# Kernel tuning notes

Hardware: AMD Instinct MI355X
Metric: run time of the kernel (lower is better)

## Reference

```python
import jax, jax.numpy as jnp
import numpy as np

N = 100000   # nodes
E = 600000   # edges
G = 64       # graphs in batch
H = 128      # hidden size
F_NODE = 2
F_EDGE = 7
RH = 500     # reghead size
NEG_SLOPE = 0.01
BN_EPS = 1e-5


def leaky(x):
    return jnp.where(x >= 0, x, NEG_SLOPE * x)


def gine_conv(x, src, dst, edge_attr, edge_W, edge_b, W1, b1, gamma, beta, W2, b2):
    # PyG GINEConv: message = ReLU(x_j + Lin(edge_attr)); sum-aggregate at dst;
    # out = nn((1+eps)*x + aggr) with eps=0; nn = Lin -> BN(train) -> LeakyReLU -> Lin -> LeakyReLU
    e = edge_attr @ edge_W.T + edge_b                 # [E, d_in]
    m = jax.nn.relu(x[src] + e)                       # gather + add + relu
    aggr = jax.ops.segment_sum(m, dst, num_segments=N)
    h = x + aggr
    h = h @ W1.T + b1                                 # [N, H]
    mu = jnp.mean(h, axis=0)
    var = jnp.var(h, axis=0)                          # biased, matches BN training
    h = gamma * (h - mu) * jax.lax.rsqrt(var + BN_EPS) + beta
    h = leaky(h)
    h = h @ W2.T + b2
    return leaky(h)


def setup_inputs() -> dict:
    key = jax.random.key(0)
    ks = jax.random.split(key, 24)

    def lin(k, out_d, in_d):
        s = 1.0 / np.sqrt(in_d)
        k1, k2 = jax.random.split(k)
        return (jax.random.uniform(k1, (out_d, in_d), jnp.float32, -s, s),
                jax.random.uniform(k2, (out_d,), jnp.float32, -s, s))

    x = jax.random.normal(ks[0], (N, F_NODE), jnp.float32)
    edge_index = jax.random.randint(ks[1], (2, E), 0, N, jnp.int32)
    batch = jnp.sort(jax.random.randint(ks[2], (N,), 0, G, jnp.int32))
    edge_attr = jax.random.normal(ks[3], (E, F_EDGE), jnp.float32)

    # layer 0 (in_dim = F_NODE)
    ew0, eb0 = lin(ks[4], F_NODE, F_EDGE)
    w10, b10 = lin(ks[5], H, F_NODE)
    g0, be0 = jnp.ones((H,), jnp.float32), jnp.zeros((H,), jnp.float32)
    w20, b20 = lin(ks[6], H, H)

    # 3 hidden layers, stacked (in_dim = H)
    L = 3
    ewS = jnp.stack([lin(ks[7 + i], H, F_EDGE)[0] for i in range(L)])
    ebS = jnp.stack([lin(jax.random.fold_in(ks[7 + i], 1), H, F_EDGE)[1] for i in range(L)])
    w1S = jnp.stack([lin(ks[10 + i], H, H)[0] for i in range(L)])
    b1S = jnp.stack([lin(jax.random.fold_in(ks[10 + i], 1), H, H)[1] for i in range(L)])
    gS = jnp.ones((L, H), jnp.float32)
    beS = jnp.zeros((L, H), jnp.float32)
    w2S = jnp.stack([lin(ks[13 + i], H, H)[0] for i in range(L)])
    b2S = jnp.stack([lin(jax.random.fold_in(ks[13 + i], 1), H, H)[1] for i in range(L)])

    wr, br = lin(ks[16], RH, H)
    we, be_ = lin(ks[17], 1, RH)

    return {"x": x, "edge_index": edge_index, "batch": batch, "edge_attr": edge_attr,
            "ew0": ew0, "eb0": eb0, "w10": w10, "b10": b10, "g0": g0, "be0": be0,
            "w20": w20, "b20": b20,
            "ewS": ewS, "ebS": ebS, "w1S": w1S, "b1S": b1S, "gS": gS, "beS": beS,
            "w2S": w2S, "b2S": b2S, "wr": wr, "br": br, "we": we, "be_": be_}


def reference(x, edge_index, batch, edge_attr,
              ew0, eb0, w10, b10, g0, be0, w20, b20,
              ewS, ebS, w1S, b1S, gS, beS, w2S, b2S,
              wr, br, we, be_):
    src, dst = edge_index[0], edge_index[1]
    h = gine_conv(x, src, dst, edge_attr, ew0, eb0, w10, b10, g0, be0, w20, b20)
    h = leaky(h)  # outer self.relu; dropout p=0 is identity
    for i in range(ewS.shape[0]):
        h = gine_conv(h, src, dst, edge_attr, ewS[i], ebS[i], w1S[i], b1S[i],
                      gS[i], beS[i], w2S[i], b2S[i])
        h = leaky(h)
    # global_mean_pool
    sums = jax.ops.segment_sum(h, batch, num_segments=G)
    cnt = jax.ops.segment_sum(jnp.ones((h.shape[0],), h.dtype), batch, num_segments=G)
    pooled = sums / jnp.maximum(cnt, 1.0)[:, None]
    # reghead_layers == 2
    r = leaky(pooled @ wr.T + br)
    return r @ we.T + be_
```

## Files before the change

### kernel.cpp

```cpp
#include <hip/hip_runtime.h>

#define NNODES 100000
#define NEDGES 600000
#define NGRAPH 64
#define HID 128
#define RHD 500
#define NB ((NNODES + 255) / 256)
#define EB ((NEDGES + 255) / 256)
#define GG ((NNODES + 63) / 64)

typedef __attribute__((ext_vector_type(8))) short short8;
typedef __attribute__((ext_vector_type(4))) float f32x4;

__device__ __forceinline__ float leaky1(float x) { return x >= 0.0f ? x : 0.01f * x; }

__device__ __forceinline__ void splitf(float a, unsigned short& h, unsigned short& l)
{
    unsigned u = __float_as_uint(a);
    unsigned r = (u + 0x7FFFu + ((u >> 16) & 1u)) & 0xFFFF0000u;
    h = (unsigned short)(r >> 16);
    float res = a - __uint_as_float(r);
    unsigned u2 = __float_as_uint(res);
    l = (unsigned short)((u2 + 0x7FFFu + ((u2 >> 16) & 1u)) >> 16);
}

__global__ __launch_bounds__(256) void hist_kernel(
    const int* __restrict__ ei, int* __restrict__ deg)
{
    int e = blockIdx.x * 256 + threadIdx.x;
    if (e < NEDGES) atomicAdd(&deg[ei[NEDGES + e]], 1);
}

__global__ __launch_bounds__(256) void scan_blk(
    const int* __restrict__ deg, int* __restrict__ incl, int* __restrict__ bsum)
{
    __shared__ int s[256];
    int t = threadIdx.x;
    int n = blockIdx.x * 256 + t;
    int v = (n < NNODES) ? deg[n] : 0;
    int x = v;
    s[t] = x;
    __syncthreads();
    for (int off = 1; off < 256; off <<= 1) {
        int y = (t >= off) ? s[t - off] : 0;
        __syncthreads();
        x += y; s[t] = x;
        __syncthreads();
    }
    if (n < NNODES) incl[n] = x;
    if (t == 255) bsum[blockIdx.x] = x;
}

__global__ __launch_bounds__(512) void scan_bsum(int* __restrict__ bsum, int nblk)
{
    __shared__ int s[512];
    int t = threadIdx.x;
    int v = (t < nblk) ? bsum[t] : 0;
    int x = v;
    s[t] = x;
    __syncthreads();
    for (int off = 1; off < 512; off <<= 1) {
        int y = (t >= off) ? s[t - off] : 0;
        __syncthreads();
        x += y; s[t] = x;
        __syncthreads();
    }
    if (t < nblk) bsum[t] = x - v;
}

__global__ __launch_bounds__(256) void finalize_rp(
    const int* __restrict__ deg, const int* __restrict__ bsum,
    int* __restrict__ rp, int* __restrict__ cursor)
{
    int n = blockIdx.x * 256 + threadIdx.x;
    if (n >= NNODES) return;
    int ig = rp[n] + bsum[blockIdx.x];
    int st = ig - deg[n];
    rp[n] = st;
    cursor[n] = st;
    if (n == NNODES - 1) rp[NNODES] = ig;
}

__global__ __launch_bounds__(256) void scatter_kernel(
    const int* __restrict__ ei, int* __restrict__ cursor, int* __restrict__ eid)
{
    int e = blockIdx.x * 256 + threadIdx.x;
    if (e >= NEDGES) return;
    int d = ei[NEDGES + e];
    int pos = atomicAdd(&cursor[d], 1);
    eid[pos] = e;
}

__global__ __launch_bounds__(256) void seg_sort(
    const int* __restrict__ rp, int* __restrict__ eid)
{
    int n = blockIdx.x * 256 + threadIdx.x;
    if (n >= NNODES) return;
    int beg = rp[n], end = rp[n + 1];
    for (int i = beg + 1; i < end; ++i) {
        int key = eid[i];
        int j = i - 1;
        while (j >= beg && eid[j] > key) { eid[j + 1] = eid[j]; --j; }
        eid[j + 1] = key;
    }
}

__global__ __launch_bounds__(256) void permute_kernel(
    const int* __restrict__ eid, const int* __restrict__ ei,
    const float* __restrict__ ea, int* __restrict__ srcp, float* __restrict__ eap)
{
    int p = blockIdx.x * 256 + threadIdx.x;
    if (p >= NEDGES) return;
    int id = eid[p];
    srcp[p] = ei[id];
    const float* s = ea + (size_t)id * 7;
    float* d = eap + (size_t)p * 7;
#pragma unroll
    for (int k = 0; k < 7; ++k) d[k] = s[k];
}

__global__ __launch_bounds__(256) void wsplit_all(
    const float* __restrict__ w20, const float* __restrict__ w1S,
    const float* __restrict__ w2S,
    unsigned short* __restrict__ wh, unsigned short* __restrict__ wl)
{
    int i = blockIdx.x * 256 + threadIdx.x;
    int m = i >> 14;
    int off = i & 16383;
    const float* src;
    if (m == 0) src = w20;
    else if (m <= 3) src = w1S + (size_t)(m - 1) * 16384;
    else src = w2S + (size_t)(m - 4) * 16384;
    unsigned short h, l;
    splitf(src[off], h, l);
    wh[i] = h;
    wl[i] = l;
}

__global__ __launch_bounds__(256) void aggregate0_kernel(
    const float* __restrict__ x, const int* __restrict__ rp,
    const int* __restrict__ srcp, const float* __restrict__ eap,
    const float* __restrict__ ew, const float* __restrict__ eb,
    float* __restrict__ aggr2)
{
    int n = blockIdx.x * 256 + threadIdx.x;
    if (n >= NNODES) return;
    float w0[7], w1[7];
#pragma unroll
    for (int k = 0; k < 7; ++k) { w0[k] = ew[k]; w1[k] = ew[7 + k]; }
    float e0b = eb[0], e1b = eb[1];
    float a0 = x[n * 2 + 0], a1 = x[n * 2 + 1];
    int beg = rp[n], end = rp[n + 1];
    for (int e = beg; e < end; ++e) {
        int s = srcp[e];
        const float* ap = eap + (size_t)e * 7;
        float t0 = e0b, t1 = e1b;
#pragma unroll
        for (int k = 0; k < 7; ++k) {
            float av = ap[k];
            t0 = fmaf(av, w0[k], t0);
            t1 = fmaf(av, w1[k], t1);
        }
        a0 += fmaxf(x[s * 2 + 0] + t0, 0.0f);
        a1 += fmaxf(x[s * 2 + 1] + t1, 0.0f);
    }
    aggr2[n * 2 + 0] = a0;
    aggr2[n * 2 + 1] = a1;
}

__global__ __launch_bounds__(256) void aggregate_kernel(
    const float* __restrict__ hin, const int* __restrict__ rp,
    const int* __restrict__ srcp, const float* __restrict__ eap,
    const float* __restrict__ ew, const float* __restrict__ eb,
    unsigned short* __restrict__ Ahi, unsigned short* __restrict__ Alo)
{
    const int lane = threadIdx.x & 63;
    const int w = threadIdx.x >> 6;
    const int nbase = blockIdx.x * 32 + w * 8;
    const int nend = nbase + 8;

    float ew0[7], ew1[7];
#pragma unroll
    for (int k = 0; k < 7; ++k) {
        ew0[k] = ew[lane * 7 + k];
        ew1[k] = ew[(lane + 64) * 7 + k];
    }
    const float eb0v = eb[lane], eb1v = eb[lane + 64];

    int n = nbase;
    int e = rp[nbase];
    const int eend = rp[nend];
    int next = rp[n + 1];
    float a0 = hin[(size_t)n * HID + lane];
    float a1 = hin[(size_t)n * HID + 64 + lane];

#define EMIT_ADVANCE() { \
        unsigned short hh0, ll0, hh1, ll1; \
        splitf(a0, hh0, ll0); splitf(a1, hh1, ll1); \
        size_t rb = (size_t)n * HID; \
        Ahi[rb + lane] = hh0; Ahi[rb + 64 + lane] = hh1; \
        Alo[rb + lane] = ll0; Alo[rb + 64 + lane] = ll1; \
        ++n; \
        a0 = hin[(size_t)n * HID + lane]; \
        a1 = hin[(size_t)n * HID + 64 + lane]; \
        next = rp[n + 1]; }

    while (e + 4 <= eend) {
        int s0 = srcp[e], s1 = srcp[e + 1], s2 = srcp[e + 2], s3 = srcp[e + 3];
        const float* ap = eap + (size_t)e * 7;
        float x00 = hin[(size_t)s0 * HID + lane];
        float x01 = hin[(size_t)s0 * HID + 64 + lane];
        float x10 = hin[(size_t)s1 * HID + lane];
        float x11 = hin[(size_t)s1 * HID + 64 + lane];
        float x20 = hin[(size_t)s2 * HID + lane];
        float x21 = hin[(size_t)s2 * HID + 64 + lane];
        float x30 = hin[(size_t)s3 * HID + lane];
        float x31 = hin[(size_t)s3 * HID + 64 + lane];
        float t00 = eb0v, t01 = eb1v, t10 = eb0v, t11 = eb1v;
        float t20 = eb0v, t21 = eb1v, t30 = eb0v, t31 = eb1v;
#pragma unroll
        for (int k = 0; k < 7; ++k) {
            float av0 = ap[k], av1 = ap[7 + k], av2 = ap[14 + k], av3 = ap[21 + k];
            t00 = fmaf(av0, ew0[k], t00); t01 = fmaf(av0, ew1[k], t01);
            t10 = fmaf(av1, ew0[k], t10); t11 = fmaf(av1, ew1[k], t11);
            t20 = fmaf(av2, ew0[k], t20); t21 = fmaf(av2, ew1[k], t21);
            t30 = fmaf(av3, ew0[k], t30); t31 = fmaf(av3, ew1[k], t31);
        }
        float m00 = fmaxf(x00 + t00, 0.0f), m01 = fmaxf(x01 + t01, 0.0f);
        float m10 = fmaxf(x10 + t10, 0.0f), m11 = fmaxf(x11 + t11, 0.0f);
        float m20 = fmaxf(x20 + t20, 0.0f), m21 = fmaxf(x21 + t21, 0.0f);
        float m30 = fmaxf(x30 + t30, 0.0f), m31 = fmaxf(x31 + t31, 0.0f);
        while (e >= next)     EMIT_ADVANCE();
        a0 += m00; a1 += m01;
        while (e + 1 >= next) EMIT_ADVANCE();
        a0 += m10; a1 += m11;
        while (e + 2 >= next) EMIT_ADVANCE();
        a0 += m20; a1 += m21;
        while (e + 3 >= next) EMIT_ADVANCE();
        a0 += m30; a1 += m31;
        e += 4;
    }
    for (; e < eend; ++e) {
        int s = srcp[e];
        const float* ap = eap + (size_t)e * 7;
        float xv0 = hin[(size_t)s * HID + lane];
        float xv1 = hin[(size_t)s * HID + 64 + lane];
        float t0 = eb0v, t1 = eb1v;
#pragma unroll
        for (int k = 0; k < 7; ++k) {
            float av = ap[k];
            t0 = fmaf(av, ew0[k], t0);
            t1 = fmaf(av, ew1[k], t1);
        }
        while (e >= next) EMIT_ADVANCE();
        a0 += fmaxf(xv0 + t0, 0.0f);
        a1 += fmaxf(xv1 + t1, 0.0f);
    }
#undef EMIT_ADVANCE
    while (n < nend) {
        unsigned short hh0, ll0, hh1, ll1;
        splitf(a0, hh0, ll0); splitf(a1, hh1, ll1);
        size_t rb = (size_t)n * HID;
        Ahi[rb + lane] = hh0; Ahi[rb + 64 + lane] = hh1;
        Alo[rb + lane] = ll0; Alo[rb + 64 + lane] = ll1;
        ++n;
        if (n < nend) {
            a0 = hin[(size_t)n * HID + lane];
            a1 = hin[(size_t)n * HID + 64 + lane];
            next = rp[n + 1];
        }
    }
}

__global__ __launch_bounds__(256) void gemm1_l0_kernel(
    const float* __restrict__ aggr2,
    const float* __restrict__ w1, const float* __restrict__ b1,
    float* __restrict__ h1)
{
    int n = blockIdx.x * 256 + threadIdx.x;
    if (n >= NNODES) return;
    float x0 = aggr2[n * 2 + 0];
    float x1 = aggr2[n * 2 + 1];
    float4* out4 = (float4*)(h1 + (size_t)n * HID);
    for (int j = 0; j < HID; j += 4) {
        float4 o;
        o.x = fmaf(x1, w1[(j + 0) * 2 + 1], fmaf(x0, w1[(j + 0) * 2 + 0], b1[j + 0]));
        o.y = fmaf(x1, w1[(j + 1) * 2 + 1], fmaf(x0, w1[(j + 1) * 2 + 0], b1[j + 1]));
        o.z = fmaf(x1, w1[(j + 2) * 2 + 1], fmaf(x0, w1[(j + 2) * 2 + 0], b1[j + 2]));
        o.w = fmaf(x1, w1[(j + 3) * 2 + 1], fmaf(x0, w1[(j + 3) * 2 + 0], b1[j + 3]));
        out4[j >> 2] = o;
    }
}

__global__ __launch_bounds__(256) void bn_stats_part(
    const float* __restrict__ h1, float* __restrict__ part)
{
    __shared__ float ls[HID], lq[HID];
    int c = threadIdx.x & 127;
    int half = threadIdx.x >> 7;
    int base = blockIdx.x * 256;
    int end = base + 256; if (end > NNODES) end = NNODES;
    float s = 0.0f, q = 0.0f;
    for (int r = base + half; r < end; r += 2) {
        float v = h1[(size_t)r * HID + c];
        s += v;
        q = fmaf(v, v, q);
    }
    if (half) { ls[c] = s; lq[c] = q; }
    __syncthreads();
    if (!half) {
        s += ls[c]; q += lq[c];
        part[(size_t)blockIdx.x * 256 + c] = s;
        part[(size_t)blockIdx.x * 256 + 128 + c] = q;
    }
}

__global__ __launch_bounds__(256) void bn_finalize(
    const float* __restrict__ part, int nblk,
    const float* __restrict__ gamma, const float* __restrict__ beta,
    float* __restrict__ scsh)
{
    __shared__ float ls[256], lq[256];
    int c = blockIdx.x;
    int t = threadIdx.x;
    float s = 0.0f, q = 0.0f;
    for (int i = t; i < nblk; i += 256) {
        s += part[(size_t)i * 256 + c];
        q += part[(size_t)i * 256 + 128 + c];
    }
    ls[t] = s; lq[t] = q;
    __syncthreads();
#pragma unroll
    for (int off = 128; off >= 1; off >>= 1) {
        if (t < off) { ls[t] += ls[t + off]; lq[t] += lq[t + off]; }
        __syncthreads();
    }
    if (t == 0) {
        const float invN = 1.0f / (float)NNODES;
        float mu = ls[0] * invN;
        float var = fmaf(-mu, mu, lq[0] * invN);
        float iv = rsqrtf(var + 1e-5f);
        float sc = gamma[c] * iv;
        scsh[c] = sc;
        scsh[HID + c] = beta[c] - mu * sc;
    }
}

__global__ __launch_bounds__(256) void gemm1_lds(
    const unsigned short* __restrict__ Ahi, const unsigned short* __restrict__ Alo,
    const unsigned short* __restrict__ wh, const unsigned short* __restrict__ wl,
    const float* __restrict__ b1, float* __restrict__ h1,
    float* __restrict__ part)
{
    __shared__ __align__(16) short lds[16384];
    const int t = threadIdx.x;
    const int mb = blockIdx.x * 64;

#pragma unroll
    for (int u = 0; u < 4; ++u) {
        int idx = u * 256 + t;
        int row = idx >> 4, sl = idx & 15;
        int gr = mb + row;
        short8 hv, lv;
#pragma unroll
        for (int e = 0; e < 8; ++e) { hv[e] = 0; lv[e] = 0; }
        if (gr < NNODES) {
            hv = *(const short8*)(Ahi + (size_t)gr * HID + sl * 8);
            lv = *(const short8*)(Alo + (size_t)gr * HID + sl * 8);
        }
        int byt = row * 256 + ((sl ^ (row & 7)) << 4);
        *(short8*)((char*)lds + byt) = hv;
        *(short8*)((char*)lds + 16384 + byt) = lv;
    }
    __syncthreads();

    const int lane = t & 63;
    const int wv = t >> 6;
    const int cl = lane & 15, g = lane >> 4, x = lane & 7;
    const int colbase = wv * 32;

    int aoff[4];
#pragma unroll
    for (int ks = 0; ks < 4; ++ks)
        aoff[ks] = cl * 256 + (((ks * 4 + g) ^ x) << 4);

    const unsigned short* wb_h0 = wh + (size_t)(colbase + cl) * HID + g * 8;
    const unsigned short* wb_h1 = wb_h0 + 16 * HID;
    const unsigned short* wb_l0 = wl + (size_t)(colbase + cl) * HID + g * 8;
    const unsigned short* wb_l1 = wb_l0 + 16 * HID;

    f32x4 acc[4][2];
#pragma unroll
    for (int rt = 0; rt < 4; ++rt) {
        acc[rt][0] = (f32x4){0.f, 0.f, 0.f, 0.f};
        acc[rt][1] = (f32x4){0.f, 0.f, 0.f, 0.f};
    }

#pragma unroll
    for (int ks = 0; ks < 4; ++ks) {
        short8 bh0 = *(const short8*)(wb_h0 + ks * 32);
        short8 bh1 = *(const short8*)(wb_h1 + ks * 32);
        short8 bl0 = *(const short8*)(wb_l0 + ks * 32);
        short8 bl1 = *(const short8*)(wb_l1 + ks * 32);
#pragma unroll
        for (int rt = 0; rt < 4; ++rt) {
            short8 ah = *(const short8*)((const char*)lds + (rt * 4096) + aoff[ks]);
            short8 al = *(const short8*)((const char*)lds + (16384 + rt * 4096) + aoff[ks]);
            acc[rt][0] = __builtin_amdgcn_mfma_f32_16x16x32_bf16(ah, bh0, acc[rt][0], 0, 0, 0);
            acc[rt][1] = __builtin_amdgcn_mfma_f32_16x16x32_bf16(ah, bh1, acc[rt][1], 0, 0, 0);
            acc[rt][0] = __builtin_amdgcn_mfma_f32_16x16x32_bf16(al, bh0, acc[rt][0], 0, 0, 0);
            acc[rt][1] = __builtin_amdgcn_mfma_f32_16x16x32_bf16(al, bh1, acc[rt][1], 0, 0, 0);
            acc[rt][0] = __builtin_amdgcn_mfma_f32_16x16x32_bf16(ah, bl0, acc[rt][0], 0, 0, 0);
            acc[rt][1] = __builtin_amdgcn_mfma_f32_16x16x32_bf16(ah, bl1, acc[rt][1], 0, 0, 0);
        }
    }

    float bj0 = b1[colbase + cl];
    float bj1 = b1[colbase + 16 + cl];
    float s0 = 0.f, q0 = 0.f, s1 = 0.f, q1 = 0.f;
#pragma unroll
    for (int rt = 0; rt < 4; ++rt) {
        int rbase = mb + rt * 16 + g * 4;
#pragma unroll
        for (int r = 0; r < 4; ++r) {
            int grow = rbase + r;
            if (grow < NNODES) {
                float o0 = acc[rt][0][r] + bj0;
                float o1 = acc[rt][1][r] + bj1;
                h1[(size_t)grow * HID + colbase + cl] = o0;
                h1[(size_t)grow * HID + colbase + 16 + cl] = o1;
                s0 += o0; q0 = fmaf(o0, o0, q0);
                s1 += o1; q1 = fmaf(o1, o1, q1);
            }
        }
    }
    __syncthreads();
    float* red = (float*)lds;
    red[(colbase + cl) * 4 + g] = s0;
    red[(colbase + 16 + cl) * 4 + g] = s1;
    red[512 + (colbase + cl) * 4 + g] = q0;
    red[512 + (colbase + 16 + cl) * 4 + g] = q1;
    __syncthreads();
    {
        int stat = t >> 7, col = t & 127;
        const float* bp = red + stat * 512 + col * 4;
        part[(size_t)blockIdx.x * 256 + stat * 128 + col] = bp[0] + bp[1] + bp[2] + bp[3];
    }
}

template<int PRE, int POST>
__global__ __launch_bounds__(256) void gemm_mfma(
    const float* __restrict__ Ain, const float* __restrict__ scsh,
    const unsigned short* __restrict__ wh, const unsigned short* __restrict__ wl,
    const float* __restrict__ bias, float* __restrict__ Hout)
{
    __shared__ __align__(16) short lds[16384];
    const int t = threadIdx.x;
    const int mb = blockIdx.x * 64;

    const float4* sc4 = (const float4*)scsh;
    const float4* sh4 = (const float4*)(scsh + HID);

#pragma unroll
    for (int u = 0; u < 4; ++u) {
        int idx = u * 256 + t;
        int row = idx >> 4, sl = idx & 15;
        float4 v0 = make_float4(0.f, 0.f, 0.f, 0.f);
        float4 v1 = make_float4(0.f, 0.f, 0.f, 0.f);
        int gr = mb + row;
        if (gr < NNODES) {
            const float4* p = (const float4*)(Ain + (size_t)gr * HID + sl * 8);
            v0 = p[0]; v1 = p[1];
            if (PRE) {
                float4 c0 = sc4[sl * 2], c1 = sc4[sl * 2 + 1];
                float4 s0 = sh4[sl * 2], s1 = sh4[sl * 2 + 1];
                v0.x = leaky1(fmaf(v0.x, c0.x, s0.x));
                v0.y = leaky1(fmaf(v0.y, c0.y, s0.y));
                v0.z = leaky1(fmaf(v0.z, c0.z, s0.z));
                v0.w = leaky1(fmaf(v0.w, c0.w, s0.w));
                v1.x = leaky1(fmaf(v1.x, c1.x, s1.x));
                v1.y = leaky1(fmaf(v1.y, c1.y, s1.y));
                v1.z = leaky1(fmaf(v1.z, c1.z, s1.z));
                v1.w = leaky1(fmaf(v1.w, c1.w, s1.w));
            }
        }
        unsigned short h[8], l[8];
        splitf(v0.x, h[0], l[0]); splitf(v0.y, h[1], l[1]);
        splitf(v0.z, h[2], l[2]); splitf(v0.w, h[3], l[3]);
        splitf(v1.x, h[4], l[4]); splitf(v1.y, h[5], l[5]);
        splitf(v1.z, h[6], l[6]); splitf(v1.w, h[7], l[7]);
        short8 hv, lv;
#pragma unroll
        for (int e = 0; e < 8; ++e) { hv[e] = (short)h[e]; lv[e] = (short)l[e]; }
        int byt = row * 256 + ((sl ^ (row & 7)) << 4);
        *(short8*)((char*)lds + byt) = hv;
        *(short8*)((char*)lds + 16384 + byt) = lv;
    }
    __syncthreads();

    const int lane = t & 63;
    const int wv = t >> 6;
    const int cl = lane & 15, g = lane >> 4, x = lane & 7;
    const int colbase = wv * 32;

    int aoff[4];
#pragma unroll
    for (int ks = 0; ks < 4; ++ks)
        aoff[ks] = cl * 256 + (((ks * 4 + g) ^ x) << 4);

    const unsigned short* wb_h0 = wh + (size_t)(colbase + cl) * HID + g * 8;
    const unsigned short* wb_h1 = wb_h0 + 16 * HID;
    const unsigned short* wb_l0 = wl + (size_t)(colbase + cl) * HID + g * 8;
    const unsigned short* wb_l1 = wb_l0 + 16 * HID;

    f32x4 acc[4][2];
#pragma unroll
    for (int rt = 0; rt < 4; ++rt) {
        acc[rt][0] = (f32x4){0.f, 0.f, 0.f, 0.f};
        acc[rt][1] = (f32x4){0.f, 0.f, 0.f, 0.f};
    }

#pragma unroll
    for (int ks = 0; ks < 4; ++ks) {
        short8 bh0 = *(const short8*)(wb_h0 + ks * 32);
        short8 bh1 = *(const short8*)(wb_h1 + ks * 32);
        short8 bl0 = *(const short8*)(wb_l0 + ks * 32);
        short8 bl1 = *(const short8*)(wb_l1 + ks * 32);
#pragma unroll
        for (int rt = 0; rt < 4; ++rt) {
            short8 ah = *(const short8*)((const char*)lds + (rt * 4096) + aoff[ks]);
            short8 al = *(const short8*)((const char*)lds + (16384 + rt * 4096) + aoff[ks]);
            acc[rt][0] = __builtin_amdgcn_mfma_f32_16x16x32_bf16(ah, bh0, acc[rt][0], 0, 0, 0);
            acc[rt][1] = __builtin_amdgcn_mfma_f32_16x16x32_bf16(ah, bh1, acc[rt][1], 0, 0, 0);
            acc[rt][0] = __builtin_amdgcn_mfma_f32_16x16x32_bf16(al, bh0, acc[rt][0], 0, 0, 0);
            acc[rt][1] = __builtin_amdgcn_mfma_f32_16x16x32_bf16(al, bh1, acc[rt][1], 0, 0, 0);
            acc[rt][0] = __builtin_amdgcn_mfma_f32_16x16x32_bf16(ah, bl0, acc[rt][0], 0, 0, 0);
            acc[rt][1] = __builtin_amdgcn_mfma_f32_16x16x32_bf16(ah, bl1, acc[rt][1], 0, 0, 0);
        }
    }

    float bj0 = bias[colbase + cl];
    float bj1 = bias[colbase + 16 + cl];
#pragma unroll
    for (int rt = 0; rt < 4; ++rt) {
        int rbase = mb + rt * 16 + g * 4;
#pragma unroll
        for (int r = 0; r < 4; ++r) {
            int grow = rbase + r;
            if (grow < NNODES) {
                float o0 = acc[rt][0][r] + bj0;
                float o1 = acc[rt][1][r] + bj1;
                if (POST) { o0 = leaky1(leaky1(o0)); o1 = leaky1(leaky1(o1)); }
                Hout[(size_t)grow * HID + colbase + cl] = o0;
                Hout[(size_t)grow * HID + colbase + 16 + cl] = o1;
            }
        }
    }
}

__global__ __launch_bounds__(256) void pool_kernel(
    const float* __restrict__ h, const int* __restrict__ batch,
    float* __restrict__ sums, float* __restrict__ cnt)
{
    int c = threadIdx.x & 127;
    int half = threadIdx.x >> 7;
    int base = blockIdx.x * 128 + half * 64;
    if (base >= NNODES) return;
    int end = base + 64; if (end > NNODES) end = NNODES;
    int g = batch[base];
    float acc = 0.0f, k = 0.0f;
    for (int n = base; n < end; ++n) {
        int gn = batch[n];
        if (gn != g) {
            atomicAdd(&sums[g * HID + c], acc);
            if (c == 0) atomicAdd(&cnt[g], k);
            acc = 0.0f; k = 0.0f; g = gn;
        }
        acc += h[(size_t)n * HID + c];
        k += 1.0f;
    }
    atomicAdd(&sums[g * HID + c], acc);
    if (c == 0) atomicAdd(&cnt[g], k);
}

__global__ __launch_bounds__(512) void reghead_kernel(
    const float* __restrict__ sums, const float* __restrict__ cnt,
    const float* __restrict__ wr, const float* __restrict__ br,
    const float* __restrict__ we, const float* __restrict__ be,
    float* __restrict__ out)
{
    __shared__ float pool[8 * HID];
    __shared__ float red[8][8];
    int g0 = blockIdx.x * 8;
    for (int i = threadIdx.x; i < 8 * HID; i += 512) {
        int g = g0 + (i >> 7);
        float c = cnt[g]; c = fmaxf(c, 1.0f);
        pool[i] = sums[g * HID + (i & 127)] / c;
    }
    __syncthreads();
    int j = threadIdx.x;
    float p[8];
#pragma unroll
    for (int g = 0; g < 8; ++g) p[g] = 0.0f;
    if (j < RHD) {
        float accs[8];
        float bjv = br[j];
#pragma unroll
        for (int g = 0; g < 8; ++g) accs[g] = bjv;
        const float4* wr4 = (const float4*)(wr + (size_t)j * HID);
        const float4* pool4 = (const float4*)pool;
        for (int k = 0; k < 32; ++k) {
            float4 w = wr4[k];
#pragma unroll
            for (int g = 0; g < 8; ++g) {
                float4 pv = pool4[g * 32 + k];
                accs[g] = fmaf(w.x, pv.x, accs[g]);
                accs[g] = fmaf(w.y, pv.y, accs[g]);
                accs[g] = fmaf(w.z, pv.z, accs[g]);
                accs[g] = fmaf(w.w, pv.w, accs[g]);
            }
        }
        float wej = we[j];
#pragma unroll
        for (int g = 0; g < 8; ++g) p[g] = leaky1(accs[g]) * wej;
    }
    int lane = threadIdx.x & 63, wid = threadIdx.x >> 6;
#pragma unroll
    for (int g = 0; g < 8; ++g) {
        float v = p[g];
        v += __shfl_down(v, 32); v += __shfl_down(v, 16); v += __shfl_down(v, 8);
        v += __shfl_down(v, 4);  v += __shfl_down(v, 2);  v += __shfl_down(v, 1);
        if (lane == 0) red[g][wid] = v;
    }
    __syncthreads();
    if (threadIdx.x < 8) {
        float sv = be[0];
#pragma unroll
        for (int w = 0; w < 8; ++w) sv += red[threadIdx.x][w];
        out[g0 + threadIdx.x] = sv;
    }
}

extern "C" void kernel_launch(void* const* d_in, const int* in_sizes, int n_in,
                              void* d_out, int out_size, void* d_ws, size_t ws_size,
                              hipStream_t stream)
{
    const float* x     = (const float*)d_in[0];
    const int*   ei    = (const int*)d_in[1];
    const int*   batch = (const int*)d_in[2];
    const float* ea    = (const float*)d_in[3];
    const float* ew0   = (const float*)d_in[4];
    const float* eb0   = (const float*)d_in[5];
    const float* w10   = (const float*)d_in[6];
    const float* b10   = (const float*)d_in[7];
    const float* g0v   = (const float*)d_in[8];
    const float* be0   = (const float*)d_in[9];
    const float* w20   = (const float*)d_in[10];
    const float* b20   = (const float*)d_in[11];
    const float* ewS   = (const float*)d_in[12];
    const float* ebS   = (const float*)d_in[13];
    const float* w1S   = (const float*)d_in[14];
    const float* b1S   = (const float*)d_in[15];
    const float* gS    = (const float*)d_in[16];
    const float* beS   = (const float*)d_in[17];
    const float* w2S   = (const float*)d_in[18];
    const float* b2S   = (const float*)d_in[19];
    const float* wr    = (const float*)d_in[20];
    const float* br    = (const float*)d_in[21];
    const float* we    = (const float*)d_in[22];
    const float* be_   = (const float*)d_in[23];

    float* ws    = (float*)d_ws;
    float* buf0  = ws;
    float* buf1  = buf0 + (size_t)NNODES * HID;
    float* buf2  = buf1 + (size_t)NNODES * HID;
    unsigned short* Ahi = (unsigned short*)buf2;
    unsigned short* Alo = Ahi + (size_t)NNODES * HID;
    float* part  = buf2 + (size_t)NNODES * HID;
    float* scsh  = part + (size_t)GG * 256;
    float* sums  = scsh + 256;
    float* cnt   = sums + NGRAPH * HID;
    float* aggr2 = cnt + NGRAPH;
    float* eap   = aggr2 + (size_t)NNODES * 2;
    int*   deg    = (int*)(eap + (size_t)NEDGES * 7);
    int*   cursor = deg + NNODES;
    int*   bsum   = cursor + NNODES;
    int*   rp     = bsum + 512;
    int*   eid    = rp + NNODES + 1;
    int*   srcp   = eid + NEDGES;
    unsigned short* whA = (unsigned short*)(srcp + NEDGES);
    unsigned short* wlA = whA + 7 * 16384;
    float* out   = (float*)d_out;

    hipMemsetAsync(deg, 0, (size_t)NNODES * sizeof(int), stream);
    hist_kernel<<<EB, 256, 0, stream>>>(ei, deg);
    scan_blk<<<NB, 256, 0, stream>>>(deg, rp, bsum);
    scan_bsum<<<1, 512, 0, stream>>>(bsum, NB);
    finalize_rp<<<NB, 256, 0, stream>>>(deg, bsum, rp, cursor);
    scatter_kernel<<<EB, 256, 0, stream>>>(ei, cursor, eid);
    seg_sort<<<NB, 256, 0, stream>>>(rp, eid);
    permute_kernel<<<EB, 256, 0, stream>>>(eid, ei, ea, srcp, eap);

    wsplit_all<<<448, 256, 0, stream>>>(w20, w1S, w2S, whA, wlA);

    aggregate0_kernel<<<NB, 256, 0, stream>>>(x, rp, srcp, eap, ew0, eb0, aggr2);
    gemm1_l0_kernel<<<NB, 256, 0, stream>>>(aggr2, w10, b10, buf0);
    bn_stats_part<<<NB, 256, 0, stream>>>(buf0, part);
    bn_finalize<<<HID, 256, 0, stream>>>(part, NB, g0v, be0, scsh);
    gemm_mfma<1, 1><<<GG, 256, 0, stream>>>(buf0, scsh, whA, wlA, b20, buf1);

    for (int i = 0; i < 3; ++i) {
        aggregate_kernel<<<NNODES / 32, 256, 0, stream>>>(buf1, rp, srcp, eap,
            ewS + (size_t)i * HID * 7, ebS + (size_t)i * HID, Ahi, Alo);
        gemm1_lds<<<GG, 256, 0, stream>>>(Ahi, Alo,
            whA + (size_t)(1 + i) * 16384, wlA + (size_t)(1 + i) * 16384,
            b1S + (size_t)i * HID, buf0, part);
        bn_finalize<<<HID, 256, 0, stream>>>(part, GG,
            gS + (size_t)i * HID, beS + (size_t)i * HID, scsh);
        gemm_mfma<1, 1><<<GG, 256, 0, stream>>>(buf0, scsh,
            whA + (size_t)(4 + i) * 16384, wlA + (size_t)(4 + i) * 16384,
            b2S + (size_t)i * HID, buf1);
    }

    hipMemsetAsync(sums, 0, (size_t)(NGRAPH * HID + NGRAPH) * sizeof(float), stream);
    pool_kernel<<<(NNODES + 127) / 128, 256, 0, stream>>>(buf1, batch, sums, cnt);
    reghead_kernel<<<NGRAPH / 8, 512, 0, stream>>>(sums, cnt, wr, br, we, be_, out);
}
```

Baseline: 666.4 us.

## Fuse sort with permute, layer0 aggregate with GEMM1, use global_load_lds in gemm1

```diff
diff --git a/kernel.cpp b/kernel.cpp
--- a/kernel.cpp
+++ b/kernel.cpp
@@ -91,8 +91,10 @@
     eid[pos] = e;
 }
 
-__global__ __launch_bounds__(256) void seg_sort(
-    const int* __restrict__ rp, int* __restrict__ eid)
+__global__ __launch_bounds__(256) void seg_sort_permute(
+    const int* __restrict__ rp, int* __restrict__ eid,
+    const int* __restrict__ ei, const float* __restrict__ ea,
+    int* __restrict__ srcp, float* __restrict__ eap)
 {
     int n = blockIdx.x * 256 + threadIdx.x;
     if (n >= NNODES) return;
@@ -103,20 +105,14 @@
         while (j >= beg && eid[j] > key) { eid[j + 1] = eid[j]; --j; }
         eid[j + 1] = key;
     }
-}
-
-__global__ __launch_bounds__(256) void permute_kernel(
-    const int* __restrict__ eid, const int* __restrict__ ei,
-    const float* __restrict__ ea, int* __restrict__ srcp, float* __restrict__ eap)
-{
-    int p = blockIdx.x * 256 + threadIdx.x;
-    if (p >= NEDGES) return;
-    int id = eid[p];
-    srcp[p] = ei[id];
-    const float* s = ea + (size_t)id * 7;
-    float* d = eap + (size_t)p * 7;
-#pragma unroll
-    for (int k = 0; k < 7; ++k) d[k] = s[k];
+    for (int p = beg; p < end; ++p) {
+        int id = eid[p];
+        srcp[p] = ei[id];
+        const float* s = ea + (size_t)id * 7;
+        float* d = eap + (size_t)p * 7;
+#pragma unroll
+        for (int k = 0; k < 7; ++k) d[k] = s[k];
+    }
 }
 
 __global__ __launch_bounds__(256) void wsplit_all(
@@ -137,17 +133,18 @@
     wl[i] = l;
 }
 
-__global__ __launch_bounds__(256) void aggregate0_kernel(
+__global__ __launch_bounds__(256) void layer0_fused(
     const float* __restrict__ x, const int* __restrict__ rp,
     const int* __restrict__ srcp, const float* __restrict__ eap,
     const float* __restrict__ ew, const float* __restrict__ eb,
-    float* __restrict__ aggr2)
+    const float* __restrict__ w1, const float* __restrict__ b1,
+    float* __restrict__ h1)
 {
     int n = blockIdx.x * 256 + threadIdx.x;
     if (n >= NNODES) return;
-    float w0[7], w1[7];
-#pragma unroll
-    for (int k = 0; k < 7; ++k) { w0[k] = ew[k]; w1[k] = ew[7 + k]; }
+    float w0[7], w1e[7];
+#pragma unroll
+    for (int k = 0; k < 7; ++k) { w0[k] = ew[k]; w1e[k] = ew[7 + k]; }
     float e0b = eb[0], e1b = eb[1];
     float a0 = x[n * 2 + 0], a1 = x[n * 2 + 1];
     int beg = rp[n], end = rp[n + 1];
@@ -159,13 +156,20 @@
         for (int k = 0; k < 7; ++k) {
             float av = ap[k];
             t0 = fmaf(av, w0[k], t0);
-            t1 = fmaf(av, w1[k], t1);
+            t1 = fmaf(av, w1e[k], t1);
         }
         a0 += fmaxf(x[s * 2 + 0] + t0, 0.0f);
         a1 += fmaxf(x[s * 2 + 1] + t1, 0.0f);
     }
-    aggr2[n * 2 + 0] = a0;
-    aggr2[n * 2 + 1] = a1;
+    float4* out4 = (float4*)(h1 + (size_t)n * HID);
+    for (int j = 0; j < HID; j += 4) {
+        float4 o;
+        o.x = fmaf(a1, w1[(j + 0) * 2 + 1], fmaf(a0, w1[(j + 0) * 2 + 0], b1[j + 0]));
+        o.y = fmaf(a1, w1[(j + 1) * 2 + 1], fmaf(a0, w1[(j + 1) * 2 + 0], b1[j + 1]));
+        o.z = fmaf(a1, w1[(j + 2) * 2 + 1], fmaf(a0, w1[(j + 2) * 2 + 0], b1[j + 2]));
+        o.w = fmaf(a1, w1[(j + 3) * 2 + 1], fmaf(a0, w1[(j + 3) * 2 + 0], b1[j + 3]));
+        out4[j >> 2] = o;
+    }
 }
 
 __global__ __launch_bounds__(256) void aggregate_kernel(
@@ -272,26 +276,6 @@
     }
 }
 
-__global__ __launch_bounds__(256) void gemm1_l0_kernel(
-    const float* __restrict__ aggr2,
-    const float* __restrict__ w1, const float* __restrict__ b1,
-    float* __restrict__ h1)
-{
-    int n = blockIdx.x * 256 + threadIdx.x;
-    if (n >= NNODES) return;
-    float x0 = aggr2[n * 2 + 0];
-    float x1 = aggr2[n * 2 + 1];
-    float4* out4 = (float4*)(h1 + (size_t)n * HID);
-    for (int j = 0; j < HID; j += 4) {
-        float4 o;
-        o.x = fmaf(x1, w1[(j + 0) * 2 + 1], fmaf(x0, w1[(j + 0) * 2 + 0], b1[j + 0]));
-        o.y = fmaf(x1, w1[(j + 1) * 2 + 1], fmaf(x0, w1[(j + 1) * 2 + 0], b1[j + 1]));
-        o.z = fmaf(x1, w1[(j + 2) * 2 + 1], fmaf(x0, w1[(j + 2) * 2 + 0], b1[j + 2]));
-        o.w = fmaf(x1, w1[(j + 3) * 2 + 1], fmaf(x0, w1[(j + 3) * 2 + 0], b1[j + 3]));
-        out4[j >> 2] = o;
-    }
-}
-
 __global__ __launch_bounds__(256) void bn_stats_part(
     const float* __restrict__ h1, float* __restrict__ part)
 {
@@ -354,28 +338,31 @@
 {
     __shared__ __align__(16) short lds[16384];
     const int t = threadIdx.x;
-    const int mb = blockIdx.x * 64;
-
-#pragma unroll
-    for (int u = 0; u < 4; ++u) {
-        int idx = u * 256 + t;
-        int row = idx >> 4, sl = idx & 15;
-        int gr = mb + row;
-        short8 hv, lv;
-#pragma unroll
-        for (int e = 0; e < 8; ++e) { hv[e] = 0; lv[e] = 0; }
-        if (gr < NNODES) {
-            hv = *(const short8*)(Ahi + (size_t)gr * HID + sl * 8);
-            lv = *(const short8*)(Alo + (size_t)gr * HID + sl * 8);
-        }
-        int byt = row * 256 + ((sl ^ (row & 7)) << 4);
-        *(short8*)((char*)lds + byt) = hv;
-        *(short8*)((char*)lds + 16384 + byt) = lv;
-    }
-    __syncthreads();
-
     const int lane = t & 63;
     const int wv = t >> 6;
+    const int mb = blockIdx.x * 64;
+
+    char* ldsb = (char*)lds;
+#pragma unroll
+    for (int j = 0; j < 4; ++j) {
+        int r = wv * 16 + j * 4 + (lane >> 4);
+        int gr = mb + r;
+        int gsl = (lane & 15) ^ (r & 7);
+        if (gr < NNODES) {
+            const unsigned short* gh = Ahi + (size_t)gr * HID + gsl * 8;
+            const unsigned short* gl = Alo + (size_t)gr * HID + gsl * 8;
+            __builtin_amdgcn_global_load_lds(
+                (const __attribute__((address_space(1))) unsigned int*)gh,
+                (__attribute__((address_space(3))) unsigned int*)(ldsb + wv * 4096 + j * 1024),
+                16, 0, 0);
+            __builtin_amdgcn_global_load_lds(
+                (const __attribute__((address_space(1))) unsigned int*)gl,
+                (__attribute__((address_space(3))) unsigned int*)(ldsb + 16384 + wv * 4096 + j * 1024),
+                16, 0, 0);
+        }
+    }
+    __syncthreads();
+
     const int cl = lane & 15, g = lane >> 4, x = lane & 7;
     const int colbase = wv * 32;
 
@@ -680,8 +667,7 @@
     float* scsh  = part + (size_t)GG * 256;
     float* sums  = scsh + 256;
     float* cnt   = sums + NGRAPH * HID;
-    float* aggr2 = cnt + NGRAPH;
-    float* eap   = aggr2 + (size_t)NNODES * 2;
+    float* eap   = cnt + NGRAPH;
     int*   deg    = (int*)(eap + (size_t)NEDGES * 7);
     int*   cursor = deg + NNODES;
     int*   bsum   = cursor + NNODES;
@@ -698,13 +684,11 @@
     scan_bsum<<<1, 512, 0, stream>>>(bsum, NB);
     finalize_rp<<<NB, 256, 0, stream>>>(deg, bsum, rp, cursor);
     scatter_kernel<<<EB, 256, 0, stream>>>(ei, cursor, eid);
-    seg_sort<<<NB, 256, 0, stream>>>(rp, eid);
-    permute_kernel<<<EB, 256, 0, stream>>>(eid, ei, ea, srcp, eap);
+    seg_sort_permute<<<NB, 256, 0, stream>>>(rp, eid, ei, ea, srcp, eap);
 
     wsplit_all<<<448, 256, 0, stream>>>(w20, w1S, w2S, whA, wlA);
 
-    aggregate0_kernel<<<NB, 256, 0, stream>>>(x, rp, srcp, eap, ew0, eb0, aggr2);
-    gemm1_l0_kernel<<<NB, 256, 0, stream>>>(aggr2, w10, b10, buf0);
+    layer0_fused<<<NB, 256, 0, stream>>>(x, rp, srcp, eap, ew0, eb0, w10, b10, buf0);
     bn_stats_part<<<NB, 256, 0, stream>>>(buf0, part);
     bn_finalize<<<HID, 256, 0, stream>>>(part, NB, g0v, be0, scsh);
     gemm_mfma<1, 1><<<GG, 256, 0, stream>>>(buf0, scsh, whA, wlA, b20, buf1);
```

Measured after the change: 672.9 us. No clear change (+1.0%).
